# Optimization experiments

Measured on AMD Instinct MI355X. Metric: run time of the kernel, lower is better.

Reference implementation:

```python
import jax, jax.numpy as jnp
import numpy as np

N_FEATURES = 16
NUM_INSTANCES = 8  # labels in [0, 8); with random labels all instances present
DELTA_V = 0.5
DELTA_D = 1.5
ALPHA, BETA, GAMMA = 1.0, 1.0, 0.001
B, H, W = 16, 512, 512


def setup_inputs() -> dict:
    key = jax.random.key(0)
    k1, k2 = jax.random.split(key)
    prediction = jax.random.normal(k1, (B, N_FEATURES, H, W), dtype=jnp.float32)
    target = jax.random.randint(k2, (B, H, W), 0, NUM_INSTANCES, dtype=jnp.int64)
    return {"prediction": prediction, "target": target}


def _per_image(pred, labels):
    # pred: [F, H, W] -> [HW, F]; labels: [H, W] -> [HW]
    F = pred.shape[0]
    x = pred.reshape(F, -1).T            # [HW, F]
    lab = labels.reshape(-1)             # [HW]
    K = NUM_INSTANCES

    counts = jax.ops.segment_sum(jnp.ones_like(lab, dtype=x.dtype), lab, num_segments=K)  # [K]
    counts = jnp.maximum(counts, 1.0)
    seg_sum = jax.ops.segment_sum(x, lab, num_segments=K)  # [K, F]
    mu = seg_sum / counts[:, None]                          # [K, F] cluster means

    # l_var: intra-cluster pull
    mu_g = mu[lab]                                          # gather [HW, F]
    d = jnp.linalg.norm(mu_g - x, axis=1) - DELTA_V         # [HW]
    d = jnp.maximum(d, 0.0) ** 2
    l_var = (jax.ops.segment_sum(d, lab, num_segments=K) / counts).sum() / K

    # l_dist: inter-cluster push (pairwise, off-diagonal via 1-eye mask)
    mu_diff = jnp.linalg.norm(mu[:, None, :] - mu[None, :, :], axis=-1)  # [K, K]
    hinge = 2.0 * DELTA_D * (1.0 - jnp.eye(K, dtype=x.dtype)) - mu_diff
    l_dist = (jnp.maximum(hinge, 0.0) ** 2).sum() / K / (K - 1)

    # l_reg
    l_reg = jnp.linalg.norm(mu, axis=1).sum() / K

    loss = ALPHA * l_var + BETA * l_dist + GAMMA * l_reg
    return jnp.stack([loss, l_var, l_dist, l_reg])


def reference(prediction, target):
    per = jax.vmap(_per_image)(prediction, target)  # [B, 4]
    return per.mean(axis=0)                          # [4]: loss, l_var, l_dist, l_reg
```

## Files before the change

### kernel.cpp

```cpp
#include <hip/hip_runtime.h>
#include <hip/hip_bf16.h>

constexpr int F_ = 16;
constexpr int K_ = 8;
constexpr int B_ = 16;
constexpr int HW_ = 512 * 512;
constexpr float DELTA_V = 0.5f;
constexpr float TWO_DELTA_D = 3.0f;
constexpr float GAMMA = 0.001f;

constexpr int CHUNKS = 64;
constexpr int PIX = HW_ / CHUNKS;
constexpr int SLOT = 136;
constexpr int NPART = B_ * CHUNKS;

constexpr int OFF_PART = 0;
constexpr int OFF_MU   = OFF_PART + NPART * SLOT;
constexpr int OFF_INV  = OFF_MU + B_ * 128;
constexpr int OFF_IMG  = OFF_INV + B_ * K_;
constexpr int OFF_LVAR = OFF_IMG + 2 * B_;

__device__ inline float waveReduceSum(float v) {
#pragma unroll
  for (int off = 32; off > 0; off >>= 1)
    v += __shfl_down(v, off, 64);
  return v;
}

__device__ inline float comp(const float4& v, int i) {
  return i == 0 ? v.x : i == 1 ? v.y : i == 2 ? v.z : v.w;
}

__global__ __launch_bounds__(256) void k1_sums(const float* __restrict__ pred,
                                               const int* __restrict__ tgt,
                                               float* __restrict__ ws) {
  float* part = ws + OFF_PART;
  const int b = blockIdx.y;
  const int chunk = blockIdx.x;
  const int lane = threadIdx.x;
  const int wy = threadIdx.y;

  float acc[4][8];
#pragma unroll
  for (int j = 0; j < 4; ++j)
#pragma unroll
    for (int k = 0; k < 8; ++k) acc[j][k] = 0.f;
  float cnt[8];
#pragma unroll
  for (int k = 0; k < 8; ++k) cnt[k] = 0.f;

  const int* tb = tgt + b * HW_ + chunk * PIX;
  const float* pb = pred + (size_t)b * F_ * HW_ + chunk * PIX;

  constexpr int ITERS = PIX / 256;
#pragma unroll 1
  for (int it = 0; it < ITERS; ++it) {
    const int p = it * 256 + lane * 4;
    const int4 lb = *reinterpret_cast<const int4*>(tb + p);
    float4 xr[4];
#pragma unroll
    for (int j = 0; j < 4; ++j)
      xr[j] = *reinterpret_cast<const float4*>(pb + (wy * 4 + j) * HW_ + p);

    const int labs[4] = {lb.x, lb.y, lb.z, lb.w};
    float sel[4][8];
#pragma unroll
    for (int pp = 0; pp < 4; ++pp)
#pragma unroll
      for (int k = 0; k < 8; ++k) sel[pp][k] = (labs[pp] == k) ? 1.f : 0.f;

#pragma unroll
    for (int j = 0; j < 4; ++j) {
#pragma unroll
      for (int k = 0; k < 8; ++k) {
        acc[j][k] = fmaf(sel[0][k], xr[j].x, acc[j][k]);
        acc[j][k] = fmaf(sel[1][k], xr[j].y, acc[j][k]);
        acc[j][k] = fmaf(sel[2][k], xr[j].z, acc[j][k]);
        acc[j][k] = fmaf(sel[3][k], xr[j].w, acc[j][k]);
      }
    }
    if (wy == 0) {
#pragma unroll
      for (int k = 0; k < 8; ++k)
        cnt[k] += sel[0][k] + sel[1][k] + sel[2][k] + sel[3][k];
    }
  }

  float* slot = part + (size_t)(b * CHUNKS + chunk) * SLOT;
#pragma unroll
  for (int j = 0; j < 4; ++j)
#pragma unroll
    for (int k = 0; k < 8; ++k) {
      float v = waveReduceSum(acc[j][k]);
      if (lane == 0) slot[k * F_ + wy * 4 + j] = v;
    }
  if (wy == 0) {
#pragma unroll
    for (int k = 0; k < 8; ++k) {
      float v = waveReduceSum(cnt[k]);
      if (lane == 0) slot[128 + k] = v;
    }
  }
}

__global__ __launch_bounds__(256) void k2_mu(float* __restrict__ ws) {
  const float* part = ws + OFF_PART;
  float* invc = ws + OFF_INV;
  float* mu = ws + OFF_MU;
  float* img = ws + OFF_IMG;
  float* lvar = ws + OFF_LVAR;
  const int b = blockIdx.x, t = threadIdx.x;
  __shared__ float tot[SLOT];
  __shared__ float mu_s[8][17];
  __shared__ float inv_s[8];
  __shared__ float lreg_arr[8];

  if (t < B_ && b == 0) lvar[t] = 0.f;

  if (t < SLOT) {
    float s = 0.f;
    const float* p = part + (size_t)b * CHUNKS * SLOT + t;
    for (int c = 0; c < CHUNKS; ++c) s += p[(size_t)c * SLOT];
    tot[t] = s;
  }
  __syncthreads();
  if (t < 8) {
    float c = fmaxf(tot[128 + t], 1.f);
    float iv = 1.f / c;
    inv_s[t] = iv;
    invc[b * K_ + t] = iv;
  }
  __syncthreads();
  if (t < 128) {
    int k = t >> 4, f = t & 15;
    float m = tot[t] * inv_s[k];
    mu[b * 128 + t] = m;
    mu_s[k][f] = m;
  }
  __syncthreads();
  if (t < 8) {
    float s = 0.f;
#pragma unroll
    for (int f = 0; f < 16; ++f) s = fmaf(mu_s[t][f], mu_s[t][f], s);
    lreg_arr[t] = sqrtf(s);
  }
  if (t < 64) {
    int a = t >> 3, c2 = t & 7;
    float v = 0.f;
    if (a != c2) {
      float dsq = 0.f;
#pragma unroll
      for (int f = 0; f < 16; ++f) {
        float dd = mu_s[a][f] - mu_s[c2][f];
        dsq = fmaf(dd, dd, dsq);
      }
      float h = fmaxf(TWO_DELTA_D - sqrtf(dsq), 0.f);
      v = h * h;
    }
    v = waveReduceSum(v);
    if (t == 0) img[b * 2 + 0] = v;
  }
  __syncthreads();
  if (t == 0) {
    float lr = 0.f;
#pragma unroll
    for (int k = 0; k < 8; ++k) lr += lreg_arr[k];
    img[b * 2 + 1] = lr;
  }
}

__global__ __launch_bounds__(256) void k3_lvar(const float* __restrict__ pred,
                                               const int* __restrict__ tgt,
                                               float* __restrict__ ws) {
  const float* mu = ws + OFF_MU;
  const float* inv = ws + OFF_INV;
  float* lvar = ws + OFF_LVAR;
  const int b = blockIdx.y, chunk = blockIdx.x;
  const int t = threadIdx.x;
  __shared__ alignas(16) float mu_s[8][20];
  __shared__ float inv_s[8];
  __shared__ float red[4];
  if (t < 128) mu_s[t >> 4][t & 15] = mu[b * 128 + t];
  if (t < 8) inv_s[t] = inv[b * K_ + t];
  __syncthreads();

  const int* tb = tgt + b * HW_ + chunk * PIX;
  const float* pb = pred + (size_t)b * F_ * HW_ + chunk * PIX;

  float lsum = 0.f;
  constexpr int ITERS = PIX / 1024;
#pragma unroll 1
  for (int it = ITERS - 1; it >= 0; --it) {
    const int p = it * 1024 + t * 4;
    const int4 lb = *reinterpret_cast<const int4*>(tb + p);
    float4 xr[16];
#pragma unroll
    for (int f = 0; f < 16; ++f)
      xr[f] = *reinterpret_cast<const float4*>(pb + f * HW_ + p);

    const int labs[4] = {lb.x, lb.y, lb.z, lb.w};
    float d2[4] = {0.f, 0.f, 0.f, 0.f};
#pragma unroll
    for (int pp = 0; pp < 4; ++pp) {
      const float* mrow = &mu_s[labs[pp]][0];
#pragma unroll
      for (int f4 = 0; f4 < 4; ++f4) {
        const float4 m = *reinterpret_cast<const float4*>(mrow + f4 * 4);
        float e0 = comp(xr[f4 * 4 + 0], pp) - m.x;
        float e1 = comp(xr[f4 * 4 + 1], pp) - m.y;
        float e2 = comp(xr[f4 * 4 + 2], pp) - m.z;
        float e3 = comp(xr[f4 * 4 + 3], pp) - m.w;
        float s = fmaf(e0, e0, 0.f);
        s = fmaf(e1, e1, s);
        s = fmaf(e2, e2, s);
        s = fmaf(e3, e3, s);
        d2[pp] += s;
      }
    }
#pragma unroll
    for (int pp = 0; pp < 4; ++pp) {
      float dist = sqrtf(d2[pp]);
      float h = fmaxf(dist - DELTA_V, 0.f);
      lsum = fmaf(h * h, inv_s[labs[pp]], lsum);
    }
  }
  float v = waveReduceSum(lsum);
  const int lane = t & 63, wid = t >> 6;
  if (lane == 0) red[wid] = v;
  __syncthreads();
  if (t == 0) atomicAdd(&lvar[b], red[0] + red[1] + red[2] + red[3]);
}

__global__ void k4_final(const float* __restrict__ ws, float* __restrict__ out) {
  const float* img = ws + OFF_IMG;
  const float* lvar = ws + OFF_LVAR;
  float lv = 0.f, ld = 0.f, lr = 0.f;
#pragma unroll
  for (int b = 0; b < B_; ++b) {
    lv += lvar[b];
    ld += img[b * 2 + 0];
    lr += img[b * 2 + 1];
  }
  lv *= 1.f / (K_ * (float)B_);
  ld *= 1.f / (K_ * (K_ - 1) * (float)B_);
  lr *= 1.f / (K_ * (float)B_);
  out[0] = lv + ld + GAMMA * lr;
  out[1] = lv;
  out[2] = ld;
  out[3] = lr;
}

extern "C" void kernel_launch(void* const* d_in, const int* in_sizes, int n_in,
                              void* d_out, int out_size, void* d_ws, size_t ws_size,
                              hipStream_t stream) {
  const float* pred = (const float*)d_in[0];
  const int* tgt = (const int*)d_in[1];
  float* out = (float*)d_out;
  float* ws = (float*)d_ws;

  hipLaunchKernelGGL(k1_sums, dim3(CHUNKS, B_), dim3(64, 4), 0, stream, pred, tgt, ws);
  hipLaunchKernelGGL(k2_mu, dim3(B_), dim3(256), 0, stream, ws);
  hipLaunchKernelGGL(k3_lvar, dim3(CHUNKS, B_), dim3(256), 0, stream, pred, tgt, ws);
  hipLaunchKernelGGL(k4_final, dim3(1), dim3(1), 0, stream, ws, out);
}
```

Before: 106.5 us.

## Fuse mean computation and final reduction into the lvar kernel

Removes the separate mu kernel by having every lvar block redundantly reduce the 64 chunk partials for its image and compute the means and inverse counts in shared memory. Chunk 0 of each image also computes l_dist and l_reg. The final reduction kernel is replaced by a last-block-done atomic counter, and a memset zeroes the accumulators. This cuts two kernel launches and their serialization gaps, at the cost of each block rereading about 35KB of partials.

```diff
diff --git a/kernel.cpp b/kernel.cpp
--- a/kernel.cpp
+++ b/kernel.cpp
@@ -15,10 +15,9 @@
 constexpr int NPART = B_ * CHUNKS;
 
 constexpr int OFF_PART = 0;
-constexpr int OFF_MU   = OFF_PART + NPART * SLOT;
-constexpr int OFF_INV  = OFF_MU + B_ * 128;
-constexpr int OFF_IMG  = OFF_INV + B_ * K_;
+constexpr int OFF_IMG  = OFF_PART + NPART * SLOT;
 constexpr int OFF_LVAR = OFF_IMG + 2 * B_;
+constexpr int OFF_DONE = OFF_LVAR + B_;
 
 __device__ inline float waveReduceSum(float v) {
 #pragma unroll
@@ -103,86 +102,67 @@
   }
 }
 
-__global__ __launch_bounds__(256) void k2_mu(float* __restrict__ ws) {
+__global__ __launch_bounds__(256) void k3_lvar(const float* __restrict__ pred,
+                                               const int* __restrict__ tgt,
+                                               float* __restrict__ ws,
+                                               float* __restrict__ out) {
   const float* part = ws + OFF_PART;
-  float* invc = ws + OFF_INV;
-  float* mu = ws + OFF_MU;
-  float* img = ws + OFF_IMG;
+  float* img  = ws + OFF_IMG;
   float* lvar = ws + OFF_LVAR;
-  const int b = blockIdx.x, t = threadIdx.x;
+  unsigned* done = (unsigned*)(ws + OFF_DONE);
+  const int b = blockIdx.y, chunk = blockIdx.x;
+  const int t = threadIdx.x;
+
   __shared__ float tot[SLOT];
-  __shared__ float mu_s[8][17];
+  __shared__ alignas(16) float mu_s[8][20];
   __shared__ float inv_s[8];
-  __shared__ float lreg_arr[8];
-
-  if (t < B_ && b == 0) lvar[t] = 0.f;
+  __shared__ float red[4];
 
   if (t < SLOT) {
     float s = 0.f;
     const float* p = part + (size_t)b * CHUNKS * SLOT + t;
+#pragma unroll 8
     for (int c = 0; c < CHUNKS; ++c) s += p[(size_t)c * SLOT];
     tot[t] = s;
   }
   __syncthreads();
-  if (t < 8) {
-    float c = fmaxf(tot[128 + t], 1.f);
-    float iv = 1.f / c;
-    inv_s[t] = iv;
-    invc[b * K_ + t] = iv;
-  }
-  __syncthreads();
-  if (t < 128) {
-    int k = t >> 4, f = t & 15;
-    float m = tot[t] * inv_s[k];
-    mu[b * 128 + t] = m;
-    mu_s[k][f] = m;
-  }
-  __syncthreads();
-  if (t < 8) {
-    float s = 0.f;
-#pragma unroll
-    for (int f = 0; f < 16; ++f) s = fmaf(mu_s[t][f], mu_s[t][f], s);
-    lreg_arr[t] = sqrtf(s);
-  }
-  if (t < 64) {
-    int a = t >> 3, c2 = t & 7;
-    float v = 0.f;
-    if (a != c2) {
-      float dsq = 0.f;
-#pragma unroll
-      for (int f = 0; f < 16; ++f) {
-        float dd = mu_s[a][f] - mu_s[c2][f];
-        dsq = fmaf(dd, dd, dsq);
-      }
-      float h = fmaxf(TWO_DELTA_D - sqrtf(dsq), 0.f);
-      v = h * h;
-    }
-    v = waveReduceSum(v);
-    if (t == 0) img[b * 2 + 0] = v;
-  }
-  __syncthreads();
-  if (t == 0) {
-    float lr = 0.f;
-#pragma unroll
-    for (int k = 0; k < 8; ++k) lr += lreg_arr[k];
-    img[b * 2 + 1] = lr;
-  }
-}
-
-__global__ __launch_bounds__(256) void k3_lvar(const float* __restrict__ pred,
-                                               const int* __restrict__ tgt,
-                                               float* __restrict__ ws) {
-  const float* mu = ws + OFF_MU;
-  const float* inv = ws + OFF_INV;
-  float* lvar = ws + OFF_LVAR;
-  const int b = blockIdx.y, chunk = blockIdx.x;
-  const int t = threadIdx.x;
-  __shared__ alignas(16) float mu_s[8][20];
-  __shared__ float inv_s[8];
-  __shared__ float red[4];
-  if (t < 128) mu_s[t >> 4][t & 15] = mu[b * 128 + t];
-  if (t < 8) inv_s[t] = inv[b * K_ + t];
-  __syncthreads();
+  if (t < 8) inv_s[t] = 1.f / fmaxf(tot[128 + t], 1.f);
+  __syncthreads();
+  if (t < 128) mu_s[t >> 4][t & 15] = tot[t] * inv_s[t >> 4];
+  __syncthreads();
+
+  if (chunk == 0) {
+    __shared__ float lreg_arr[8];
+    if (t < 8) {
+      float s = 0.f;
+#pragma unroll
+      for (int f = 0; f < 16; ++f) s = fmaf(mu_s[t][f], mu_s[t][f], s);
+      lreg_arr[t] = sqrtf(s);
+    }
+    if (t < 64) {
+      int a = t >> 3, c2 = t & 7;
+      float v = 0.f;
+      if (a != c2) {
+        float dsq = 0.f;
+#pragma unroll
+        for (int f = 0; f < 16; ++f) {
+          float dd = mu_s[a][f] - mu_s[c2][f];
+          dsq = fmaf(dd, dd, dsq);
+        }
+        float h = fmaxf(TWO_DELTA_D - sqrtf(dsq), 0.f);
+        v = h * h;
+      }
+      v = waveReduceSum(v);
+      if (t == 0) img[b * 2 + 0] = v;
+    }
+    __syncthreads();
+    if (t == 0) {
+      float lr = 0.f;
+#pragma unroll
+      for (int k = 0; k < 8; ++k) lr += lreg_arr[k];
+      img[b * 2 + 1] = lr;
+    }
+  }
 
   const int* tb = tgt + b * HW_ + chunk * PIX;
   const float* pb = pred + (size_t)b * F_ * HW_ + chunk * PIX;
@@ -228,26 +208,28 @@
   const int lane = t & 63, wid = t >> 6;
   if (lane == 0) red[wid] = v;
   __syncthreads();
-  if (t == 0) atomicAdd(&lvar[b], red[0] + red[1] + red[2] + red[3]);
-}
-
-__global__ void k4_final(const float* __restrict__ ws, float* __restrict__ out) {
-  const float* img = ws + OFF_IMG;
-  const float* lvar = ws + OFF_LVAR;
-  float lv = 0.f, ld = 0.f, lr = 0.f;
-#pragma unroll
-  for (int b = 0; b < B_; ++b) {
-    lv += lvar[b];
-    ld += img[b * 2 + 0];
-    lr += img[b * 2 + 1];
-  }
-  lv *= 1.f / (K_ * (float)B_);
-  ld *= 1.f / (K_ * (K_ - 1) * (float)B_);
-  lr *= 1.f / (K_ * (float)B_);
-  out[0] = lv + ld + GAMMA * lr;
-  out[1] = lv;
-  out[2] = ld;
-  out[3] = lr;
+
+  if (t == 0) {
+    atomicAdd(&lvar[b], red[0] + red[1] + red[2] + red[3]);
+    unsigned d = __hip_atomic_fetch_add(done, 1u, __ATOMIC_ACQ_REL,
+                                        __HIP_MEMORY_SCOPE_AGENT);
+    if (d == (unsigned)(NPART - 1)) {
+      float lv = 0.f, ld = 0.f, lr = 0.f;
+#pragma unroll
+      for (int bb = 0; bb < B_; ++bb) {
+        lv += __hip_atomic_load(&lvar[bb], __ATOMIC_RELAXED, __HIP_MEMORY_SCOPE_AGENT);
+        ld += __hip_atomic_load(&img[bb * 2 + 0], __ATOMIC_RELAXED, __HIP_MEMORY_SCOPE_AGENT);
+        lr += __hip_atomic_load(&img[bb * 2 + 1], __ATOMIC_RELAXED, __HIP_MEMORY_SCOPE_AGENT);
+      }
+      lv *= 1.f / (K_ * (float)B_);
+      ld *= 1.f / (K_ * (K_ - 1) * (float)B_);
+      lr *= 1.f / (K_ * (float)B_);
+      out[0] = lv + ld + GAMMA * lr;
+      out[1] = lv;
+      out[2] = ld;
+      out[3] = lr;
+    }
+  }
 }
 
 extern "C" void kernel_launch(void* const* d_in, const int* in_sizes, int n_in,
@@ -258,8 +240,7 @@
   float* out = (float*)d_out;
   float* ws = (float*)d_ws;
 
+  hipMemsetAsync(ws + OFF_LVAR, 0, (B_ + 1) * sizeof(float), stream);
   hipLaunchKernelGGL(k1_sums, dim3(CHUNKS, B_), dim3(64, 4), 0, stream, pred, tgt, ws);
-  hipLaunchKernelGGL(k2_mu, dim3(B_), dim3(256), 0, stream, ws);
-  hipLaunchKernelGGL(k3_lvar, dim3(CHUNKS, B_), dim3(256), 0, stream, pred, tgt, ws);
-  hipLaunchKernelGGL(k4_final, dim3(1), dim3(1), 0, stream, ws, out);
-}
+  hipLaunchKernelGGL(k3_lvar, dim3(CHUNKS, B_), dim3(256), 0, stream, pred, tgt, ws, out);
+}
```

Measured after the change: 152.2 us. 43.0% more time.
